# Performance work log

Measured on AMD Instinct MI355X. Metric: run time of the kernel, lower is better.

## Reference

```python
import jax, jax.numpy as jnp
import numpy as np

B, NO, NM, NV, E = 16, 512, 128, 64, 256
H, DK, MS, FF = 16, 16, 8, 512
TRANS_MAX = 100.0


def _ln(x):
    m = x.mean(-1, keepdims=True)
    v = ((x - m) ** 2).mean(-1, keepdims=True)
    return (x - m) * jax.lax.rsqrt(v + 1e-5)


def _inv_norm(x):
    # 1 - minmax-normalize over the whole per-batch matrix
    mn = x.min(axis=(1, 2), keepdims=True)
    mx = x.max(axis=(1, 2), keepdims=True)
    return 1.0 - (x - mn) / (mx - mn)


def _adjacency(proc_time, trans_time, MVpair_trans, mask_dyn, mask_ma):
    # masked copy of proc_time
    A_proc = jnp.where(mask_dyn, proc_time, 0.0)
    # keep only the per-row minimum nonzero entry (min_ProcTime_elements)
    nz = jnp.where(A_proc == 0.0, jnp.inf, A_proc)
    mn = nz.min(axis=2, keepdims=True)
    keep = (A_proc == mn) & (A_proc != 0.0)
    A_proc = A_proc * keep.astype(proc_time.dtype)
    A_proc_norm = (A_proc > 0.0).astype(proc_time.dtype)
    # machine-machine masks
    mask2 = mask_ma[:, None, :] & mask_ma[:, :, None]  # [B, nm, nm]
    A_procing = (~mask2).astype(proc_time.dtype)
    A_off = _inv_norm(MVpair_trans)
    tt = jnp.where(mask2, trans_time, TRANS_MAX + 1.0)
    A_on = _inv_norm(tt)
    return A_proc_norm, A_procing, A_off, A_on


def _block(row, col, cost, Wq, Wk, Wv, Wo, mW1, mb1, mW2, mb2, fW1, fb1, fW2, fb2):
    # MatNet-style mixed-score multi-head attention encoding block
    Bb, R, _ = row.shape
    C = col.shape[1]
    q = (row @ Wq).reshape(Bb, R, H, DK).transpose(0, 2, 1, 3)  # bhrd
    k = (col @ Wk).reshape(Bb, C, H, DK).transpose(0, 2, 1, 3)  # bhcd
    v = (col @ Wv).reshape(Bb, C, H, DK).transpose(0, 2, 1, 3)
    dot = jnp.einsum('bhrd,bhcd->bhrc', q, k) / jnp.sqrt(jnp.asarray(DK, row.dtype))
    two = jnp.stack([dot, jnp.broadcast_to(cost[:, None], dot.shape)], axis=-1)  # [B,H,R,C,2]
    hmix = jax.nn.relu(jnp.einsum('bhrct,hts->bhrcs', two, mW1) + mb1[None, :, None, None, :])
    score = jnp.einsum('bhrcs,hso->bhrco', hmix, mW2)[..., 0] + mb2[:, 0][None, :, None, None]
    attn = jax.nn.softmax(score, axis=-1)
    ctx = jnp.einsum('bhrc,bhcd->bhrd', attn, v).transpose(0, 2, 1, 3).reshape(Bb, R, H * DK)
    out1 = _ln(row + ctx @ Wo)
    ffn = jax.nn.relu(out1 @ fW1 + fb1) @ fW2 + fb2
    return _ln(out1 + ffn)


def setup_inputs() -> dict:
    key = jax.random.key(0)
    ks = jax.random.split(key, 24)

    def nrm(i, shape, s=0.05):
        return jax.random.normal(ks[i], shape, jnp.float32) * s

    return {
        'ope_emb': nrm(0, (B, NO, E), 1.0),
        'ma_emb': nrm(1, (B, NM, E), 1.0),
        'veh_emb': nrm(2, (B, NV, E), 1.0),
        'proc_time': jax.random.uniform(ks[3], (B, NO, NM), jnp.float32) * 20.0,
        'offload_trans_time': jax.random.uniform(ks[4], (B, NO, NV), jnp.float32) * TRANS_MAX,
        'trans_time': jax.random.uniform(ks[5], (B, NM, NM), jnp.float32) * TRANS_MAX,
        'MVpair_trans': jax.random.uniform(ks[6], (B, NV, NM), jnp.float32) * TRANS_MAX,
        'mask_dyn_ope_ma_adj': jax.random.bernoulli(ks[7], 0.3, (B, NO, NM)),
        'mask_ma': jax.random.bernoulli(ks[8], 0.7, (B, NM)),
        # stacked params for the 4 blocks: 0=ope, 1=veh, 2=ma1, 3=ma2
        'Wq': nrm(9, (4, E, H * DK)),
        'Wk': nrm(10, (4, E, H * DK)),
        'Wv': nrm(11, (4, E, H * DK)),
        'Wo': nrm(12, (4, H * DK, E)),
        'mixW1': nrm(13, (4, H, 2, MS), 0.3),
        'mixb1': jnp.zeros((4, H, MS), jnp.float32),
        'mixW2': nrm(14, (4, H, MS, 1), 0.3),
        'mixb2': jnp.zeros((4, H, 1), jnp.float32),
        'ffW1': nrm(15, (4, E, FF)),
        'ffb1': jnp.zeros((4, FF), jnp.float32),
        'ffW2': nrm(16, (4, FF, E)),
        'ffb2': jnp.zeros((4, E), jnp.float32),
        'maprojW': nrm(17, (2 * E, E)),
        'maprojb': jnp.zeros((E,), jnp.float32),
    }


def reference(ope_emb, ma_emb, veh_emb, proc_time, offload_trans_time, trans_time,
              MVpair_trans, mask_dyn_ope_ma_adj, mask_ma,
              Wq, Wk, Wv, Wo, mixW1, mixb1, mixW2, mixb2,
              ffW1, ffb1, ffW2, ffb2, maprojW, maprojb):
    A_proc_norm, A_procing, A_off, A_on = _adjacency(
        proc_time, trans_time, MVpair_trans, mask_dyn_ope_ma_adj, mask_ma)

    def blk(i, row, col, cost):
        return _block(row, col, cost, Wq[i], Wk[i], Wv[i], Wo[i],
                      mixW1[i], mixb1[i], mixW2[i], mixb2[i],
                      ffW1[i], ffb1[i], ffW2[i], ffb2[i])

    ope_out = blk(0, ope_emb, ma_emb, A_proc_norm)
    veh_out = blk(1, veh_emb, ma_emb, A_off)
    ma1 = blk(2, ma_emb, ma_emb, A_procing)
    ma2 = blk(3, ma_emb, ma_emb, A_on)
    ma_out = jnp.concatenate([ma1, ma2], axis=-1) @ maprojW + maprojb
    return (ope_out, ma_out, veh_out)
```

## Files before the change

kernel.cpp:

```cpp
#include <hip/hip_runtime.h>
#include <hip/hip_fp16.h>
#include <hip/hip_bf16.h>


typedef unsigned short u16;
typedef __attribute__((ext_vector_type(8))) short bf16x8;
typedef __attribute__((ext_vector_type(4))) float f32x4;
struct us4 { u16 x, y, z, w; };

__device__ __forceinline__ float bf2f(u16 u) {
  return __uint_as_float(((unsigned int)u) << 16);
}
__device__ __forceinline__ u16 f2bf(float f) {
  unsigned int x = __float_as_uint(f);
  x += 0x7FFFu + ((x >> 16) & 1u);
  return (u16)(x >> 16);
}
__device__ __forceinline__ __half2 h2max(__half2 a, __half2 b) {
  unsigned au = *(unsigned*)&a, bu = *(unsigned*)&b, ru;
  asm("v_pk_max_f16 %0, %1, %2" : "=v"(ru) : "v"(au), "v"(bu));
  return *(__half2*)&ru;
}

#define NBATCH 16
#define NOPE   512
#define NMA    128
#define NVEH   64
#define EDIM   256

struct PrepArgs {
  const float* ope; const float* ma; const float* veh;
  u16* ope_bf; u16* ma_bf; u16* veh_bf;
  const float* proc; const int* mask_dyn; float* A_proc;
  const float* mv; const float* trans; const int* mask_ma;
  unsigned int* mm;
};
struct TrArgs {
  const float* Wq; const float* Wk; const float* Wv; const float* Wo;
  const float* ffW1; const float* ffW2; const float* maproj;
  u16* WqT; u16* WkT; u16* WvT; u16* WoT; u16* ffW1T; u16* ffW2T; u16* maprojT;
};
__global__ __launch_bounds__(256) void prep_a(PrepArgs a, TrArgs tr) {
  int blk = blockIdx.x, t = threadIdx.x;
  if (blk < 2816) {
    int i = blk * 256 + t;
    const float* s; u16* d; int j;
    if (i < 524288)      { s = a.ope; d = a.ope_bf; j = i; }
    else if (i < 655360) { s = a.ma;  d = a.ma_bf;  j = i - 524288; }
    else                 { s = a.veh; d = a.veh_bf; j = i - 655360; }
    float4 v = ((const float4*)s)[j];
    us4 o = { f2bf(v.x), f2bf(v.y), f2bf(v.z), f2bf(v.w) };
    ((us4*)d)[j] = o;
    return;
  }
  if (blk < 6912) {
    int local = blk - 2816;
    int row = local * 2 + (t >> 7);
    int lane = t & 127;
    size_t idx = (size_t)row * NMA + lane;
    float av = a.mask_dyn[idx] ? a.proc[idx] : 0.0f;
    float cand = (av != 0.0f) ? av : 1.0e30f;
    __shared__ float red[256];
    red[t] = cand;
    __syncthreads();
    for (int s = 64; s > 0; s >>= 1) {
      if (lane < s) red[t] = fminf(red[t], red[t + s]);
      __syncthreads();
    }
    float mn = red[t & 128];
    a.A_proc[idx] = (av != 0.0f && av == mn) ? 1.0f : 0.0f;
    return;
  }
  if (blk < 7104) {
    __shared__ float smn[256], smx[256];
    float mn = 1.0e30f, mx = -1.0e30f;
    int mmIdx;
    if (blk < 6976) {
      int local = blk - 6912;
      int b = local >> 2, chunk = local & 3;
      const float* xb = a.mv + (size_t)b * 8192 + chunk * 2048;
#pragma unroll
      for (int r = 0; r < 8; r++) {
        float v = xb[r * 256 + t];
        mn = fminf(mn, v);
        mx = fmaxf(mx, v);
      }
      mmIdx = b;
    } else {
      int local = blk - 6976;
      int b = local >> 3, chunk = local & 7;
      __shared__ unsigned char mrow[NMA];
      if (t < NMA) mrow[t] = (unsigned char)(a.mask_ma[(size_t)b * NMA + t] != 0);
      __syncthreads();
      const float* tb = a.trans + (size_t)b * 16384 + chunk * 2048;
      int rbase = chunk * 16;
#pragma unroll
      for (int r = 0; r < 8; r++) {
        int off = r * 256 + t;
        int row = rbase + (off >> 7), col = off & 127;
        bool m2 = mrow[row] && mrow[col];
        float tt = m2 ? tb[off] : 101.0f;
        mn = fminf(mn, tt);
        mx = fmaxf(mx, tt);
      }
      mmIdx = 16 + b;
    }
    smn[t] = mn; smx[t] = mx;
    __syncthreads();
    for (int s = 128; s > 0; s >>= 1) {
      if (t < s) {
        smn[t] = fminf(smn[t], smn[t + s]);
        smx[t] = fmaxf(smx[t], smx[t + s]);
      }
      __syncthreads();
    }
    if (t == 0) {
      atomicMin(&a.mm[mmIdx], __float_as_uint(smn[0]));
      atomicMax(&a.mm[32 + mmIdx], __float_as_uint(smx[0]));
    }
    return;
  }
  {
    int b2 = blk - 7104;
    const float* src; u16* dst; int Kd, Nd, tile;
    if (b2 < 1024) {
      int w = b2 >> 8, i = (b2 >> 6) & 3; tile = b2 & 63;
      const float* sw = (w == 0 ? tr.Wq : w == 1 ? tr.Wk : w == 2 ? tr.Wv : tr.Wo);
      u16* dw = (w == 0 ? tr.WqT : w == 1 ? tr.WkT : w == 2 ? tr.WvT : tr.WoT);
      src = sw + (size_t)i * 65536; dst = dw + (size_t)i * 65536;
      Kd = 256; Nd = 256;
    } else if (b2 < 1536) {
      int z = (b2 - 1024) >> 7; tile = (b2 - 1024) & 127;
      src = tr.ffW1 + (size_t)z * 131072; dst = tr.ffW1T + (size_t)z * 131072;
      Kd = 256; Nd = 512;
    } else {
      int z = (b2 - 1536) >> 7; tile = (b2 - 1536) & 127;
      if (z < 4) { src = tr.ffW2 + (size_t)z * 131072; dst = tr.ffW2T + (size_t)z * 131072; }
      else       { src = tr.maproj; dst = tr.maprojT; }
      Kd = 512; Nd = 256;
    }
    int nx = Nd >> 5;
    int k0 = (tile / nx) * 32, n0 = (tile % nx) * 32;
    __shared__ float tl[32][33];
    int tx = t & 31, ty = t >> 5;
#pragma unroll
    for (int r = 0; r < 4; r++)
      tl[ty + r * 8][tx] = src[(size_t)(k0 + ty + r * 8) * Nd + n0 + tx];
    __syncthreads();
#pragma unroll
    for (int r = 0; r < 4; r++)
      dst[(size_t)(n0 + ty + r * 8) * Kd + k0 + tx] = f2bf(tl[tx][ty + r * 8]);
  }
}

__global__ __launch_bounds__(256) void prep_b(
    const float* __restrict__ mv, const float* __restrict__ trans,
    const int* __restrict__ mask_ma, const unsigned int* __restrict__ mm,
    float* __restrict__ A_offb, float* __restrict__ a_on,
    float* __restrict__ a_pcing) {
  int blk = blockIdx.x, t = threadIdx.x;
  if (blk < 512) {
    int b = blk >> 5, off = (blk & 31) * 256 + t;
    float lo = __uint_as_float(mm[b]);
    float inv = 1.0f / (__uint_as_float(mm[32 + b]) - lo);
    size_t idx = (size_t)b * 8192 + off;
    A_offb[idx] = 1.0f - (mv[idx] - lo) * inv;
    return;
  }
  int local = blk - 512;
  int b = local >> 6, off = (local & 63) * 256 + t;
  int row = off >> 7, col = off & 127;
  bool m2 = (mask_ma[(size_t)b * NMA + row] != 0) &&
            (mask_ma[(size_t)b * NMA + col] != 0);
  size_t idx = (size_t)b * 16384 + off;
  float tt = m2 ? trans[idx] : 101.0f;
  float lo = __uint_as_float(mm[16 + b]);
  float inv = 1.0f / (__uint_as_float(mm[48 + b]) - lo);
  a_on[idx] = 1.0f - (tt - lo) * inv;
  a_pcing[idx] = m2 ? 0.0f : 1.0f;
}

__global__ __launch_bounds__(256) void transpose_v(
    const u16* __restrict__ src, u16* __restrict__ dst) {
  int g = blockIdx.z >> 4, b = blockIdx.z & 15;
  int d0 = blockIdx.x * 32, c0 = blockIdx.y * 32;
  __shared__ u16 tile[32][33];
  int tx = threadIdx.x & 31, ty = threadIdx.x >> 5;
  const u16* s = src + ((size_t)g * 16 + b) * 32768;
  u16* d = dst + ((size_t)g * 16 + b) * 32768;
#pragma unroll
  for (int r = 0; r < 4; r++)
    tile[ty + r * 8][tx] = s[(size_t)(c0 + ty + r * 8) * 256 + d0 + tx];
  __syncthreads();
#pragma unroll
  for (int r = 0; r < 4; r++)
    d[(size_t)(d0 + ty + r * 8) * 128 + c0 + tx] = tile[tx][ty + r * 8];
}

struct GG {
  const u16* A; const u16* WT; const float* bias; u16* C;
  int M, N, K, epi, wgStart, wgCols, mode;
};
struct GGArgs { GG g[12]; int n; };

__global__ __launch_bounds__(256) void gemm_grouped(GGArgs args) {
  int wg = blockIdx.x;
  int gi = 0;
  for (int i = 1; i < args.n; i++)
    if (wg >= args.g[i].wgStart) gi = i;
  GG gg = args.g[gi];
  int lwg = wg - gg.wgStart;
  int bx = lwg & (gg.wgCols - 1);
  int by = lwg >> ((gg.wgCols == 2) ? 1 : 2);
  int N = gg.N, K = gg.K;

  __shared__ u16 As[128][40];
  __shared__ u16 Bs[128][40];
  int tid = threadIdx.x;
  int lane = tid & 63, wid = tid >> 6;
  int wr = (wid >> 1) * 64, wc = (wid & 1) * 64;
  int m16 = lane & 15, quad = lane >> 4;
  int rb = by * 128, cb = bx * 128;
  int srow = tid >> 2;
  int schunk = (tid & 3) * 8;

  f32x4 acc[4][4];
#pragma unroll
  for (int i = 0; i < 4; i++)
#pragma unroll
    for (int j = 0; j < 4; j++) acc[i][j] = (f32x4){0.f, 0.f, 0.f, 0.f};

  for (int k0 = 0; k0 < K; k0 += 32) {
    uint4 va0 = *(const uint4*)(gg.A + (size_t)(rb + srow) * K + k0 + schunk);
    uint4 va1 = *(const uint4*)(gg.A + (size_t)(rb + 64 + srow) * K + k0 + schunk);
    uint4 vb0 = *(const uint4*)(gg.WT + (size_t)(cb + srow) * K + k0 + schunk);
    uint4 vb1 = *(const uint4*)(gg.WT + (size_t)(cb + 64 + srow) * K + k0 + schunk);
    __syncthreads();
    *(uint4*)&As[srow][schunk] = va0;
    *(uint4*)&As[64 + srow][schunk] = va1;
    *(uint4*)&Bs[srow][schunk] = vb0;
    *(uint4*)&Bs[64 + srow][schunk] = vb1;
    __syncthreads();
    bf16x8 af[4], bfr[4];
#pragma unroll
    for (int i = 0; i < 4; i++)
      af[i] = *(const bf16x8*)&As[wr + i * 16 + m16][quad * 8];
#pragma unroll
    for (int j = 0; j < 4; j++)
      bfr[j] = *(const bf16x8*)&Bs[wc + j * 16 + m16][quad * 8];
#pragma unroll
    for (int i = 0; i < 4; i++)
#pragma unroll
      for (int j = 0; j < 4; j++)
        acc[i][j] = __builtin_amdgcn_mfma_f32_16x16x32_bf16(
            af[i], bfr[j], acc[i][j], 0, 0, 0);
  }

#pragma unroll
  for (int i = 0; i < 4; i++) {
#pragma unroll
    for (int j = 0; j < 4; j++) {
      int col = cb + wc + j * 16 + m16;
      float bv = (gg.epi >= 1) ? gg.bias[col] : 0.0f;
#pragma unroll
      for (int r = 0; r < 4; r++) {
        int row = rb + wr + i * 16 + quad * 4 + r;
        float v = acc[i][j][r] + bv;
        if (gg.epi == 2) v = fmaxf(v, 0.0f);
        size_t off;
        if (gg.mode == 0) {
          off = (size_t)row * N + col;
        } else if (gg.mode == 1) {
          off = ((size_t)(row >> 4)) * 4096 + (size_t)(col >> 4) * 256 +
                (size_t)(row & 15) * 16 + (col & 15);
        } else {
          off = ((size_t)(row >> 7)) * 32768 + (size_t)(col >> 4) * 2048 +
                (size_t)(row & 127) * 16 + (col & 15);
        }
        gg.C[off] = f2bf(v);
      }
    }
  }
}

__global__ __launch_bounds__(256) void gemm_mfma_f32(
    const u16* __restrict__ A, const u16* __restrict__ WT,
    const float* __restrict__ bias, float* __restrict__ C,
    int M, int N, int K) {
  __shared__ u16 As[64][40];
  __shared__ u16 Bs[64][40];
  int tid = threadIdx.x;
  int lane = tid & 63, wid = tid >> 6;
  int wr = (wid >> 1) * 32, wc = (wid & 1) * 32;
  int m16 = lane & 15, quad = lane >> 4;
  int rb = blockIdx.y * 64, cb = blockIdx.x * 64;
  int srow = tid >> 2;
  int schunk = (tid & 3) * 8;
  f32x4 acc[2][2];
#pragma unroll
  for (int i = 0; i < 2; i++)
#pragma unroll
    for (int j = 0; j < 2; j++) acc[i][j] = (f32x4){0.f, 0.f, 0.f, 0.f};
  for (int k0 = 0; k0 < K; k0 += 32) {
    uint4 va = *(const uint4*)(A + (size_t)(rb + srow) * K + k0 + schunk);
    uint4 vb = *(const uint4*)(WT + (size_t)(cb + srow) * K + k0 + schunk);
    __syncthreads();
    *(uint4*)&As[srow][schunk] = va;
    *(uint4*)&Bs[srow][schunk] = vb;
    __syncthreads();
    bf16x8 af[2], bfr[2];
#pragma unroll
    for (int i = 0; i < 2; i++)
      af[i] = *(const bf16x8*)&As[wr + i * 16 + m16][quad * 8];
#pragma unroll
    for (int j = 0; j < 2; j++)
      bfr[j] = *(const bf16x8*)&Bs[wc + j * 16 + m16][quad * 8];
#pragma unroll
    for (int i = 0; i < 2; i++)
#pragma unroll
      for (int j = 0; j < 2; j++)
        acc[i][j] = __builtin_amdgcn_mfma_f32_16x16x32_bf16(
            af[i], bfr[j], acc[i][j], 0, 0, 0);
  }
#pragma unroll
  for (int i = 0; i < 2; i++)
#pragma unroll
    for (int j = 0; j < 2; j++) {
      int col = cb + wc + j * 16 + m16;
      float bv = bias[col];
#pragma unroll
      for (int r = 0; r < 4; r++) {
        int row = rb + wr + i * 16 + quad * 4 + r;
        C[(size_t)row * N + col] = acc[i][j][r] + bv;
      }
    }
}

struct AG {
  const u16* q; const u16* k; const u16* vT; const float* cost; u16* ctx;
  const float* w1; const float* b1; const float* w2; const float* b2;
  int R, wgStart;
};
struct AGArgs { AG g[4]; };

#define CSTRIDE 134

__global__ __launch_bounds__(256) void attn_grouped(AGArgs args) {
  int blk = blockIdx.x;
  int gi = 0;
#pragma unroll
  for (int i = 1; i < 4; i++)
    if (blk >= args.g[i].wgStart) gi = i;
  AG gg = args.g[gi];
  int local = blk - gg.wgStart;

  int t = threadIdx.x;
  int wave = t >> 6, lane = t & 63;
  int quad = lane >> 4, l16 = lane & 15;
  int j = local & 15;
  int b = (j & 7) * 2 + (j >> 3);
  int hgrp = (local >> 4) & 1;
  int tile = local >> 5;
  int m0 = b * gg.R + tile * 16;

  __shared__ __half costs_h[16 * CSTRIDE];
  __shared__ u16 pbuf[4][16 * 136];

  const float* cp = gg.cost + (size_t)m0 * 128;
  for (int i = t; i < 2048; i += 256)
    costs_h[(i >> 7) * CSTRIDE + (i & 127)] = __float2half(cp[i]);
  __syncthreads();

  const bf16x8 zerof = (bf16x8){0, 0, 0, 0, 0, 0, 0, 0};
  const f32x4 zacc = (f32x4){0.f, 0.f, 0.f, 0.f};
  const __half2 zh = __float2half2_rn(0.0f);
  u16* pb = pbuf[wave];
  const u16* qtile = gg.q + ((size_t)(m0 >> 4)) * 4096;
  const u16* kb    = gg.k + (size_t)b * 32768;

#pragma unroll
  for (int hh = 0; hh < 2; hh++) {
    int h = hgrp * 8 + wave * 2 + hh;

    __half2 w10h[8], w11h[8], b1h[8], w2h[8];
#pragma unroll
    for (int s = 0; s < 8; s++) {
      w10h[s] = __float2half2_rn(gg.w1[h * 16 + s] * 0.25f);
      w11h[s] = __float2half2_rn(gg.w1[h * 16 + 8 + s]);
      b1h[s]  = __float2half2_rn(gg.b1[h * 8 + s]);
      w2h[s]  = __float2half2_rn(gg.w2[h * 8 + s]);
    }
    float wb2v = gg.b2[h];

    bf16x8 bq = zerof;
    if (quad < 2)
      bq = *(const bf16x8*)(qtile + (size_t)h * 256 + l16 * 16 + quad * 8);
    f32x4 st[8];
    __builtin_amdgcn_s_setprio(1);
#pragma unroll
    for (int ct = 0; ct < 8; ct++) {
      bf16x8 ak = zerof;
      if (quad < 2)
        ak = *(const bf16x8*)(kb + (size_t)h * 2048 + (ct * 16 + l16) * 16 +
                              quad * 8);
      st[ct] = __builtin_amdgcn_mfma_f32_16x16x32_bf16(ak, bq, zacc, 0, 0, 0);
    }
    __builtin_amdgcn_s_setprio(0);

#pragma unroll
    for (int ct = 0; ct < 8; ct++) {
#pragma unroll
      for (int p = 0; p < 2; p++) {
        __half2 d2 = __float22half2_rn(
            make_float2(st[ct][p * 2], st[ct][p * 2 + 1]));
        __half2 c2 = *(const __half2*)&costs_h[l16 * CSTRIDE + ct * 16 +
                                               quad * 4 + p * 2];
        __half2 s2 = zh;
#pragma unroll
        for (int s = 0; s < 8; s++) {
          __half2 hm = __hfma2(d2, w10h[s], __hfma2(c2, w11h[s], b1h[s]));
          hm = h2max(hm, zh);
          s2 = __hfma2(hm, w2h[s], s2);
        }
        float2 sf = __half22float2(s2);
        st[ct][p * 2]     = sf.x + wb2v;
        st[ct][p * 2 + 1] = sf.y + wb2v;
      }
    }

    float mx = -1.0e30f;
#pragma unroll
    for (int ct = 0; ct < 8; ct++)
#pragma unroll
      for (int rg = 0; rg < 4; rg++) mx = fmaxf(mx, st[ct][rg]);
    mx = fmaxf(mx, __shfl_xor(mx, 16, 64));
    mx = fmaxf(mx, __shfl_xor(mx, 32, 64));
    float sum = 0.0f;
#pragma unroll
    for (int ct = 0; ct < 8; ct++)
#pragma unroll
      for (int rg = 0; rg < 4; rg++) {
        float e = __expf(st[ct][rg] - mx);
        st[ct][rg] = e;
        sum += e;
      }
    sum += __shfl_xor(sum, 16, 64);
    sum += __shfl_xor(sum, 32, 64);
    float inv = 1.0f / sum;

#pragma unroll
    for (int ct = 0; ct < 8; ct++) {
#pragma unroll
      for (int p = 0; p < 2; p++) {
        __hip_bfloat162 pk = __float22bfloat162_rn(
            make_float2(st[ct][p * 2] * inv, st[ct][p * 2 + 1] * inv));
        *(unsigned int*)&pb[l16 * 136 + ct * 16 + quad * 4 + p * 2] =
            *(unsigned int*)&pk;
      }
    }

    f32x4 cacc = zacc;
    __builtin_amdgcn_s_setprio(1);
#pragma unroll
    for (int ks = 0; ks < 4; ks++) {
      bf16x8 ap = *(const bf16x8*)&pb[l16 * 136 + ks * 32 + quad * 8];
      bf16x8 bv = *(const bf16x8*)(gg.vT + (size_t)b * 32768 +
                                   (size_t)(h * 16 + l16) * 128 + ks * 32 +
                                   quad * 8);
      cacc = __builtin_amdgcn_mfma_f32_16x16x32_bf16(ap, bv, cacc, 0, 0, 0);
    }
    __builtin_amdgcn_s_setprio(0);

#pragma unroll
    for (int rg = 0; rg < 4; rg++)
      gg.ctx[(size_t)(m0 + quad * 4 + rg) * 256 + h * 16 + l16] =
          f2bf(cacc[rg]);
  }
}

struct LN1Args {
  const float* r0; const float* r1; const float* r2; const float* r3;
  int s1, s2, s3;
};
__global__ __launch_bounds__(256) void ln1_grouped(
    LN1Args a, const u16* __restrict__ x, u16* __restrict__ out) {
  int row = blockIdx.x * 4 + (threadIdx.x >> 6);
  int lane = threadIdx.x & 63;
  const float* resid;
  int local;
  if (row < a.s1)      { resid = a.r0; local = row; }
  else if (row < a.s2) { resid = a.r1; local = row - a.s1; }
  else if (row < a.s3) { resid = a.r2; local = row - a.s2; }
  else                 { resid = a.r3; local = row - a.s3; }
  float4 rv = *(const float4*)(resid + (size_t)local * 256 + lane * 4);
  us4 xv = *(const us4*)(x + (size_t)row * 256 + lane * 4);
  float v0 = rv.x + bf2f(xv.x);
  float v1 = rv.y + bf2f(xv.y);
  float v2 = rv.z + bf2f(xv.z);
  float v3 = rv.w + bf2f(xv.w);
  float s  = v0 + v1 + v2 + v3;
  float ss = v0 * v0 + v1 * v1 + v2 * v2 + v3 * v3;
#pragma unroll
  for (int d = 1; d < 64; d <<= 1) {
    s  += __shfl_xor(s, d, 64);
    ss += __shfl_xor(ss, d, 64);
  }
  float mean = s * (1.0f / 256.0f);
  float var = ss * (1.0f / 256.0f) - mean * mean;
  float rs = rsqrtf(fmaxf(var, 0.0f) + 1e-5f);
  us4 o = { f2bf((v0 - mean) * rs), f2bf((v1 - mean) * rs),
            f2bf((v2 - mean) * rs), f2bf((v3 - mean) * rs) };
  *(us4*)(out + (size_t)row * 256 + lane * 4) = o;
}

struct LN2Args {
  float* f0; float* f1; u16* b2; u16* b3;
  int s1, s2, s3;
};
__global__ __launch_bounds__(256) void ln2_grouped(
    LN2Args a, const u16* __restrict__ resid, const u16* __restrict__ x) {
  int row = blockIdx.x * 4 + (threadIdx.x >> 6);
  int lane = threadIdx.x & 63;
  us4 rv = *(const us4*)(resid + (size_t)row * 256 + lane * 4);
  us4 xv = *(const us4*)(x + (size_t)row * 256 + lane * 4);
  float v0 = bf2f(rv.x) + bf2f(xv.x);
  float v1 = bf2f(rv.y) + bf2f(xv.y);
  float v2 = bf2f(rv.z) + bf2f(xv.z);
  float v3 = bf2f(rv.w) + bf2f(xv.w);
  float s  = v0 + v1 + v2 + v3;
  float ss = v0 * v0 + v1 * v1 + v2 * v2 + v3 * v3;
#pragma unroll
  for (int d = 1; d < 64; d <<= 1) {
    s  += __shfl_xor(s, d, 64);
    ss += __shfl_xor(ss, d, 64);
  }
  float mean = s * (1.0f / 256.0f);
  float var = ss * (1.0f / 256.0f) - mean * mean;
  float rs = rsqrtf(fmaxf(var, 0.0f) + 1e-5f);
  float y0 = (v0 - mean) * rs, y1 = (v1 - mean) * rs;
  float y2 = (v2 - mean) * rs, y3 = (v3 - mean) * rs;
  if (row < a.s1) {
    float4 o = {y0, y1, y2, y3};
    *(float4*)(a.f0 + (size_t)row * 256 + lane * 4) = o;
  } else if (row < a.s2) {
    float4 o = {y0, y1, y2, y3};
    *(float4*)(a.f1 + (size_t)(row - a.s1) * 256 + lane * 4) = o;
  } else if (row < a.s3) {
    us4 o = { f2bf(y0), f2bf(y1), f2bf(y2), f2bf(y3) };
    *(us4*)(a.b2 + (size_t)(row - a.s2) * 512 + lane * 4) = o;
  } else {
    us4 o = { f2bf(y0), f2bf(y1), f2bf(y2), f2bf(y3) };
    *(us4*)(a.b3 + (size_t)(row - a.s3) * 512 + 256 + lane * 4) = o;
  }
}

extern "C" void kernel_launch(void* const* d_in, const int* in_sizes, int n_in,
                              void* d_out, int out_size, void* d_ws, size_t ws_size,
                              hipStream_t stream) {
  const float* ope   = (const float*)d_in[0];
  const float* ma    = (const float*)d_in[1];
  const float* veh   = (const float*)d_in[2];
  const float* proc  = (const float*)d_in[3];
  const float* trans = (const float*)d_in[5];
  const float* mv    = (const float*)d_in[6];
  const int* mask_dyn = (const int*)d_in[7];
  const int* mask_ma  = (const int*)d_in[8];
  const float* Wq = (const float*)d_in[9];
  const float* Wk = (const float*)d_in[10];
  const float* Wv = (const float*)d_in[11];
  const float* Wo = (const float*)d_in[12];
  const float* mixW1 = (const float*)d_in[13];
  const float* mixb1 = (const float*)d_in[14];
  const float* mixW2 = (const float*)d_in[15];
  const float* mixb2 = (const float*)d_in[16];
  const float* ffW1 = (const float*)d_in[17];
  const float* ffb1 = (const float*)d_in[18];
  const float* ffW2 = (const float*)d_in[19];
  const float* ffb2 = (const float*)d_in[20];
  const float* maprojW = (const float*)d_in[21];
  const float* maprojb = (const float*)d_in[22];
  float* out = (float*)d_out;
  char* ws = (char*)d_ws;

  const int OFF[4] = {0, 8192, 9216, 11264};
  const int MS4[4] = {8192, 1024, 2048, 2048};
  const int TOT = 13312;

  const size_t MB = 1 << 20;
  float* A_proc  = (float*)(ws + 0);
  float* A_offb  = (float*)(ws + 4 * MB);
  float* A_pcing = (float*)(ws + 4 * MB + MB / 2);
  float* A_on    = (float*)(ws + 5 * MB + MB / 2);
  u16* ope_bf  = (u16*)(ws + 6 * MB + MB / 2);
  u16* ma_bf   = (u16*)(ws + 10 * MB + MB / 2);
  u16* veh_bf  = (u16*)(ws + 11 * MB + MB / 2);
  u16* WqT     = (u16*)(ws + 12 * MB);
  u16* WkT     = (u16*)(ws + 12 * MB + MB / 2);
  u16* WvT     = (u16*)(ws + 13 * MB);
  u16* WoT     = (u16*)(ws + 13 * MB + MB / 2);
  u16* ffW1T   = (u16*)(ws + 14 * MB);
  u16* ffW2T   = (u16*)(ws + 15 * MB);
  u16* maprojT = (u16*)(ws + 16 * MB);
  u16* q_all   = (u16*)(ws + 16 * MB + MB / 2);
  u16* k_all   = (u16*)(ws + 23 * MB);
  u16* v_all   = (u16*)(ws + 27 * MB);
  u16* vT_all  = (u16*)(ws + 31 * MB);
  u16* ctx_all = (u16*)(ws + 35 * MB);
  u16* t1_all  = (u16*)(ws + 41 * MB + MB / 2);
  u16* out1_all= (u16*)(ws + 48 * MB);
  u16* ffh_all = (u16*)(ws + 54 * MB + MB / 2);
  u16* maCat   = (u16*)(ws + 67 * MB + MB / 2);
  unsigned int* mmbuf = (unsigned int*)(ws + 70 * MB);

  hipMemsetAsync(mmbuf, 0x7F, 128, stream);
  hipMemsetAsync((char*)mmbuf + 128, 0x00, 128, stream);

  {
    PrepArgs pa = {ope, ma, veh, ope_bf, ma_bf, veh_bf,
                   proc, mask_dyn, A_proc, mv, trans, mask_ma, mmbuf};
    TrArgs ta = {Wq, Wk, Wv, Wo, ffW1, ffW2, maprojW,
                 WqT, WkT, WvT, WoT, ffW1T, ffW2T, maprojT};
    prep_a<<<9280, 256, 0, stream>>>(pa, ta);
  }

  prep_b<<<1536, 256, 0, stream>>>(mv, trans, mask_ma, mmbuf,
                                   A_offb, A_on, A_pcing);

  const size_t MA_OUT  = (size_t)NBATCH * NOPE * EDIM;
  const size_t VEH_OUT = MA_OUT + (size_t)NBATCH * NMA * EDIM;

  const u16* rowbf[4] = {ope_bf, veh_bf, ma_bf, ma_bf};
  const float* costp[4] = {A_proc, A_offb, A_pcing, A_on};

  {
    GGArgs ga; ga.n = 12;
    int wg = 0;
    for (int i = 0; i < 4; i++) {
      ga.g[i] = {rowbf[i], WqT + (size_t)i * 65536, nullptr,
                 q_all + (size_t)OFF[i] * 256, MS4[i], 256, 256, 0, wg, 2, 1};
      wg += (MS4[i] / 128) * 2;
    }
    for (int i = 0; i < 4; i++) {
      ga.g[4 + i] = {ma_bf, WkT + (size_t)i * 65536, nullptr,
                     k_all + (size_t)i * 524288, 2048, 256, 256, 0, wg, 2, 2};
      wg += 32;
    }
    for (int i = 0; i < 4; i++) {
      ga.g[8 + i] = {ma_bf, WvT + (size_t)i * 65536, nullptr,
                     v_all + (size_t)i * 524288, 2048, 256, 256, 0, wg, 2, 0};
      wg += 32;
    }
    gemm_grouped<<<wg, 256, 0, stream>>>(ga);
  }

  transpose_v<<<dim3(8, 4, 64), 256, 0, stream>>>(v_all, vT_all);

  {
    AGArgs aa;
    int wg = 0;
    const int R4[4] = {NOPE, NVEH, NMA, NMA};
    for (int i = 0; i < 4; i++) {
      aa.g[i] = {q_all + (size_t)OFF[i] * 256, k_all + (size_t)i * 524288,
                 vT_all + (size_t)i * 524288, costp[i],
                 ctx_all + (size_t)OFF[i] * 256,
                 mixW1 + (size_t)i * 256, mixb1 + (size_t)i * 128,
                 mixW2 + (size_t)i * 128, mixb2 + (size_t)i * 16,
                 R4[i], wg};
      wg += MS4[i] / 8;
    }
    attn_grouped<<<wg, 256, 0, stream>>>(aa);
  }

  {
    GGArgs ga; ga.n = 4;
    int wg = 0;
    for (int i = 0; i < 4; i++) {
      ga.g[i] = {ctx_all + (size_t)OFF[i] * 256, WoT + (size_t)i * 65536,
                 nullptr, t1_all + (size_t)OFF[i] * 256,
                 MS4[i], 256, 256, 0, wg, 2, 0};
      wg += (MS4[i] / 128) * 2;
    }
    gemm_grouped<<<wg, 256, 0, stream>>>(ga);
  }

  {
    LN1Args la = {ope, veh, ma, ma, 8192, 9216, 11264};
    ln1_grouped<<<TOT / 4, 256, 0, stream>>>(la, t1_all, out1_all);
  }

  {
    GGArgs ga; ga.n = 4;
    int wg = 0;
    for (int i = 0; i < 4; i++) {
      ga.g[i] = {out1_all + (size_t)OFF[i] * 256, ffW1T + (size_t)i * 131072,
                 ffb1 + (size_t)i * 512, ffh_all + (size_t)OFF[i] * 512,
                 MS4[i], 512, 256, 2, wg, 4, 0};
      wg += (MS4[i] / 128) * 4;
    }
    gemm_grouped<<<wg, 256, 0, stream>>>(ga);
  }

  {
    GGArgs ga; ga.n = 4;
    int wg = 0;
    for (int i = 0; i < 4; i++) {
      ga.g[i] = {ffh_all + (size_t)OFF[i] * 512, ffW2T + (size_t)i * 131072,
                 ffb2 + (size_t)i * 256, t1_all + (size_t)OFF[i] * 256,
                 MS4[i], 256, 512, 1, wg, 2, 0};
      wg += (MS4[i] / 128) * 2;
    }
    gemm_grouped<<<wg, 256, 0, stream>>>(ga);
  }

  {
    LN2Args la = {out, out + VEH_OUT, maCat, maCat, 8192, 9216, 11264};
    ln2_grouped<<<TOT / 4, 256, 0, stream>>>(la, out1_all, t1_all);
  }

  gemm_mfma_f32<<<dim3(4, 32), 256, 0, stream>>>(maCat, maprojT, maprojb,
      out + MA_OUT, 2048, 256, 512);
}
```

Before: 250.7 us.

## Fold prep_b and V transpose into grouped GEMM, switch to 64x64 tiles

The grouped GEMM now uses 64x64 output tiles with a 128-wide K chunk per shared-memory stage, replacing the 128x128 tile with 32-wide K steps. This gives more workgroups and fewer barriers per K. The V projection writes its transposed layout directly from the epilogue, which removes the transpose_v kernel and the intermediate v_all buffer. The prep_b cost-matrix work runs as extra workgroups appended to the first grouped GEMM launch, and the final maproj GEMM reuses the grouped kernel with a float-output mode. Together these remove three launches, at the price of less register-level reuse per tile and scattered 8-byte writes for V.

Result: slower. 354.8 us (+41.5%).

```diff
diff --git a/kernel.cpp b/kernel.cpp
--- a/kernel.cpp
+++ b/kernel.cpp
@@ -153,187 +153,135 @@
   }
 }
 
-__global__ __launch_bounds__(256) void prep_b(
-    const float* __restrict__ mv, const float* __restrict__ trans,
-    const int* __restrict__ mask_ma, const unsigned int* __restrict__ mm,
-    float* __restrict__ A_offb, float* __restrict__ a_on,
-    float* __restrict__ a_pcing) {
-  int blk = blockIdx.x, t = threadIdx.x;
+struct PB {
+  const float* mv; const float* trans; const int* mask_ma;
+  const unsigned int* mm; float* A_offb; float* a_on; float* a_pcing;
+};
+__device__ __forceinline__ void prep_b_body(const PB& p, int blk, int t) {
   if (blk < 512) {
     int b = blk >> 5, off = (blk & 31) * 256 + t;
-    float lo = __uint_as_float(mm[b]);
-    float inv = 1.0f / (__uint_as_float(mm[32 + b]) - lo);
+    float lo = __uint_as_float(p.mm[b]);
+    float inv = 1.0f / (__uint_as_float(p.mm[32 + b]) - lo);
     size_t idx = (size_t)b * 8192 + off;
-    A_offb[idx] = 1.0f - (mv[idx] - lo) * inv;
+    p.A_offb[idx] = 1.0f - (p.mv[idx] - lo) * inv;
     return;
   }
   int local = blk - 512;
   int b = local >> 6, off = (local & 63) * 256 + t;
   int row = off >> 7, col = off & 127;
-  bool m2 = (mask_ma[(size_t)b * NMA + row] != 0) &&
-            (mask_ma[(size_t)b * NMA + col] != 0);
+  bool m2 = (p.mask_ma[(size_t)b * NMA + row] != 0) &&
+            (p.mask_ma[(size_t)b * NMA + col] != 0);
   size_t idx = (size_t)b * 16384 + off;
-  float tt = m2 ? trans[idx] : 101.0f;
-  float lo = __uint_as_float(mm[16 + b]);
-  float inv = 1.0f / (__uint_as_float(mm[48 + b]) - lo);
-  a_on[idx] = 1.0f - (tt - lo) * inv;
-  a_pcing[idx] = m2 ? 0.0f : 1.0f;
-}
-
-__global__ __launch_bounds__(256) void transpose_v(
-    const u16* __restrict__ src, u16* __restrict__ dst) {
-  int g = blockIdx.z >> 4, b = blockIdx.z & 15;
-  int d0 = blockIdx.x * 32, c0 = blockIdx.y * 32;
-  __shared__ u16 tile[32][33];
-  int tx = threadIdx.x & 31, ty = threadIdx.x >> 5;
-  const u16* s = src + ((size_t)g * 16 + b) * 32768;
-  u16* d = dst + ((size_t)g * 16 + b) * 32768;
-#pragma unroll
-  for (int r = 0; r < 4; r++)
-    tile[ty + r * 8][tx] = s[(size_t)(c0 + ty + r * 8) * 256 + d0 + tx];
-  __syncthreads();
-#pragma unroll
-  for (int r = 0; r < 4; r++)
-    d[(size_t)(d0 + ty + r * 8) * 128 + c0 + tx] = tile[tx][ty + r * 8];
+  float tt = m2 ? p.trans[idx] : 101.0f;
+  float lo = __uint_as_float(p.mm[16 + b]);
+  float inv = 1.0f / (__uint_as_float(p.mm[48 + b]) - lo);
+  p.a_on[idx] = 1.0f - (tt - lo) * inv;
+  p.a_pcing[idx] = m2 ? 0.0f : 1.0f;
 }
 
 struct GG {
   const u16* A; const u16* WT; const float* bias; u16* C;
-  int M, N, K, epi, wgStart, wgCols, mode;
+  int M, N, K, epi, wgStart, cshift, mode;
 };
-struct GGArgs { GG g[12]; int n; };
+struct GGArgs { GG g[12]; PB pb; int n; int nGemmWG; };
 
 __global__ __launch_bounds__(256) void gemm_grouped(GGArgs args) {
   int wg = blockIdx.x;
+  if (wg >= args.nGemmWG) {
+    prep_b_body(args.pb, wg - args.nGemmWG, threadIdx.x);
+    return;
+  }
   int gi = 0;
   for (int i = 1; i < args.n; i++)
     if (wg >= args.g[i].wgStart) gi = i;
   GG gg = args.g[gi];
   int lwg = wg - gg.wgStart;
-  int bx = lwg & (gg.wgCols - 1);
-  int by = lwg >> ((gg.wgCols == 2) ? 1 : 2);
+  int bx = lwg & ((1 << gg.cshift) - 1);
+  int by = lwg >> gg.cshift;
   int N = gg.N, K = gg.K;
 
-  __shared__ u16 As[128][40];
-  __shared__ u16 Bs[128][40];
-  int tid = threadIdx.x;
-  int lane = tid & 63, wid = tid >> 6;
-  int wr = (wid >> 1) * 64, wc = (wid & 1) * 64;
-  int m16 = lane & 15, quad = lane >> 4;
-  int rb = by * 128, cb = bx * 128;
-  int srow = tid >> 2;
-  int schunk = (tid & 3) * 8;
-
-  f32x4 acc[4][4];
-#pragma unroll
-  for (int i = 0; i < 4; i++)
-#pragma unroll
-    for (int j = 0; j < 4; j++) acc[i][j] = (f32x4){0.f, 0.f, 0.f, 0.f};
-
-  for (int k0 = 0; k0 < K; k0 += 32) {
-    uint4 va0 = *(const uint4*)(gg.A + (size_t)(rb + srow) * K + k0 + schunk);
-    uint4 va1 = *(const uint4*)(gg.A + (size_t)(rb + 64 + srow) * K + k0 + schunk);
-    uint4 vb0 = *(const uint4*)(gg.WT + (size_t)(cb + srow) * K + k0 + schunk);
-    uint4 vb1 = *(const uint4*)(gg.WT + (size_t)(cb + 64 + srow) * K + k0 + schunk);
-    __syncthreads();
-    *(uint4*)&As[srow][schunk] = va0;
-    *(uint4*)&As[64 + srow][schunk] = va1;
-    *(uint4*)&Bs[srow][schunk] = vb0;
-    *(uint4*)&Bs[64 + srow][schunk] = vb1;
-    __syncthreads();
-    bf16x8 af[4], bfr[4];
-#pragma unroll
-    for (int i = 0; i < 4; i++)
-      af[i] = *(const bf16x8*)&As[wr + i * 16 + m16][quad * 8];
-#pragma unroll
-    for (int j = 0; j < 4; j++)
-      bfr[j] = *(const bf16x8*)&Bs[wc + j * 16 + m16][quad * 8];
-#pragma unroll
-    for (int i = 0; i < 4; i++)
-#pragma unroll
-      for (int j = 0; j < 4; j++)
-        acc[i][j] = __builtin_amdgcn_mfma_f32_16x16x32_bf16(
-            af[i], bfr[j], acc[i][j], 0, 0, 0);
-  }
-
-#pragma unroll
-  for (int i = 0; i < 4; i++) {
-#pragma unroll
-    for (int j = 0; j < 4; j++) {
-      int col = cb + wc + j * 16 + m16;
-      float bv = (gg.epi >= 1) ? gg.bias[col] : 0.0f;
-#pragma unroll
-      for (int r = 0; r < 4; r++) {
-        int row = rb + wr + i * 16 + quad * 4 + r;
-        float v = acc[i][j][r] + bv;
-        if (gg.epi == 2) v = fmaxf(v, 0.0f);
-        size_t off;
-        if (gg.mode == 0) {
-          off = (size_t)row * N + col;
-        } else if (gg.mode == 1) {
-          off = ((size_t)(row >> 4)) * 4096 + (size_t)(col >> 4) * 256 +
-                (size_t)(row & 15) * 16 + (col & 15);
-        } else {
-          off = ((size_t)(row >> 7)) * 32768 + (size_t)(col >> 4) * 2048 +
-                (size_t)(row & 127) * 16 + (col & 15);
-        }
-        gg.C[off] = f2bf(v);
-      }
-    }
-  }
-}
-
-__global__ __launch_bounds__(256) void gemm_mfma_f32(
-    const u16* __restrict__ A, const u16* __restrict__ WT,
-    const float* __restrict__ bias, float* __restrict__ C,
-    int M, int N, int K) {
-  __shared__ u16 As[64][40];
-  __shared__ u16 Bs[64][40];
+  __shared__ u16 As[64][136];
+  __shared__ u16 Bs[64][136];
   int tid = threadIdx.x;
   int lane = tid & 63, wid = tid >> 6;
   int wr = (wid >> 1) * 32, wc = (wid & 1) * 32;
   int m16 = lane & 15, quad = lane >> 4;
-  int rb = blockIdx.y * 64, cb = blockIdx.x * 64;
+  int rb = by * 64, cb = bx * 64;
   int srow = tid >> 2;
   int schunk = (tid & 3) * 8;
+
   f32x4 acc[2][2];
 #pragma unroll
   for (int i = 0; i < 2; i++)
 #pragma unroll
     for (int j = 0; j < 2; j++) acc[i][j] = (f32x4){0.f, 0.f, 0.f, 0.f};
-  for (int k0 = 0; k0 < K; k0 += 32) {
-    uint4 va = *(const uint4*)(A + (size_t)(rb + srow) * K + k0 + schunk);
-    uint4 vb = *(const uint4*)(WT + (size_t)(cb + srow) * K + k0 + schunk);
+
+  for (int kc = 0; kc < K; kc += 128) {
+    uint4 va[4], vb[4];
+    const u16* ap = gg.A + (size_t)(rb + srow) * K + kc + schunk;
+    const u16* bp = gg.WT + (size_t)(cb + srow) * K + kc + schunk;
+#pragma unroll
+    for (int c = 0; c < 4; c++) {
+      va[c] = *(const uint4*)(ap + c * 32);
+      vb[c] = *(const uint4*)(bp + c * 32);
+    }
     __syncthreads();
-    *(uint4*)&As[srow][schunk] = va;
-    *(uint4*)&Bs[srow][schunk] = vb;
+#pragma unroll
+    for (int c = 0; c < 4; c++) {
+      *(uint4*)&As[srow][c * 32 + schunk] = va[c];
+      *(uint4*)&Bs[srow][c * 32 + schunk] = vb[c];
+    }
     __syncthreads();
-    bf16x8 af[2], bfr[2];
-#pragma unroll
-    for (int i = 0; i < 2; i++)
-      af[i] = *(const bf16x8*)&As[wr + i * 16 + m16][quad * 8];
-#pragma unroll
-    for (int j = 0; j < 2; j++)
-      bfr[j] = *(const bf16x8*)&Bs[wc + j * 16 + m16][quad * 8];
-#pragma unroll
-    for (int i = 0; i < 2; i++)
-#pragma unroll
-      for (int j = 0; j < 2; j++)
-        acc[i][j] = __builtin_amdgcn_mfma_f32_16x16x32_bf16(
-            af[i], bfr[j], acc[i][j], 0, 0, 0);
-  }
-#pragma unroll
-  for (int i = 0; i < 2; i++)
+#pragma unroll
+    for (int ks = 0; ks < 4; ks++) {
+      bf16x8 af0 = *(const bf16x8*)&As[wr + m16][ks * 32 + quad * 8];
+      bf16x8 af1 = *(const bf16x8*)&As[wr + 16 + m16][ks * 32 + quad * 8];
+      bf16x8 bf0 = *(const bf16x8*)&Bs[wc + m16][ks * 32 + quad * 8];
+      bf16x8 bf1 = *(const bf16x8*)&Bs[wc + 16 + m16][ks * 32 + quad * 8];
+      acc[0][0] = __builtin_amdgcn_mfma_f32_16x16x32_bf16(af0, bf0, acc[0][0], 0, 0, 0);
+      acc[0][1] = __builtin_amdgcn_mfma_f32_16x16x32_bf16(af0, bf1, acc[0][1], 0, 0, 0);
+      acc[1][0] = __builtin_amdgcn_mfma_f32_16x16x32_bf16(af1, bf0, acc[1][0], 0, 0, 0);
+      acc[1][1] = __builtin_amdgcn_mfma_f32_16x16x32_bf16(af1, bf1, acc[1][1], 0, 0, 0);
+    }
+  }
+
+#pragma unroll
+  for (int i = 0; i < 2; i++) {
 #pragma unroll
     for (int j = 0; j < 2; j++) {
       int col = cb + wc + j * 16 + m16;
-      float bv = bias[col];
-#pragma unroll
-      for (int r = 0; r < 4; r++) {
-        int row = rb + wr + i * 16 + quad * 4 + r;
-        C[(size_t)row * N + col] = acc[i][j][r] + bv;
+      float bv = (gg.epi >= 1) ? gg.bias[col] : 0.0f;
+      if (gg.mode == 3) {
+        int row0 = rb + wr + i * 16 + quad * 4;
+        int b = row0 >> 7, c0 = row0 & 127;
+        us4 o = { f2bf(acc[i][j][0]), f2bf(acc[i][j][1]),
+                  f2bf(acc[i][j][2]), f2bf(acc[i][j][3]) };
+        *(us4*)(gg.C + (size_t)b * 32768 + (size_t)col * 128 + c0) = o;
+      } else {
+#pragma unroll
+        for (int r = 0; r < 4; r++) {
+          int row = rb + wr + i * 16 + quad * 4 + r;
+          float v = acc[i][j][r] + bv;
+          if (gg.epi == 2) v = fmaxf(v, 0.0f);
+          if (gg.mode == 4) {
+            ((float*)gg.C)[(size_t)row * N + col] = v;
+          } else {
+            size_t off;
+            if (gg.mode == 0) {
+              off = (size_t)row * N + col;
+            } else if (gg.mode == 1) {
+              off = ((size_t)(row >> 4)) * 4096 + (size_t)(col >> 4) * 256 +
+                    (size_t)(row & 15) * 16 + (col & 15);
+            } else {
+              off = ((size_t)(row >> 7)) * 32768 + (size_t)(col >> 4) * 2048 +
+                    (size_t)(row & 127) * 16 + (col & 15);
+            }
+            gg.C[off] = f2bf(v);
+          }
+        }
       }
     }
+  }
 }
 
 struct AG {
@@ -603,7 +551,6 @@
   u16* maprojT = (u16*)(ws + 16 * MB);
   u16* q_all   = (u16*)(ws + 16 * MB + MB / 2);
   u16* k_all   = (u16*)(ws + 23 * MB);
-  u16* v_all   = (u16*)(ws + 27 * MB);
   u16* vT_all  = (u16*)(ws + 31 * MB);
   u16* ctx_all = (u16*)(ws + 35 * MB);
   u16* t1_all  = (u16*)(ws + 41 * MB + MB / 2);
@@ -623,37 +570,34 @@
     prep_a<<<9280, 256, 0, stream>>>(pa, ta);
   }
 
-  prep_b<<<1536, 256, 0, stream>>>(mv, trans, mask_ma, mmbuf,
-                                   A_offb, A_on, A_pcing);
-
   const size_t MA_OUT  = (size_t)NBATCH * NOPE * EDIM;
   const size_t VEH_OUT = MA_OUT + (size_t)NBATCH * NMA * EDIM;
 
   const u16* rowbf[4] = {ope_bf, veh_bf, ma_bf, ma_bf};
   const float* costp[4] = {A_proc, A_offb, A_pcing, A_on};
-
-  {
-    GGArgs ga; ga.n = 12;
+  PB pb = {mv, trans, mask_ma, mmbuf, A_offb, A_on, A_pcing};
+
+  {
+    GGArgs ga; ga.n = 12; ga.pb = pb;
     int wg = 0;
     for (int i = 0; i < 4; i++) {
       ga.g[i] = {rowbf[i], WqT + (size_t)i * 65536, nullptr,
                  q_all + (size_t)OFF[i] * 256, MS4[i], 256, 256, 0, wg, 2, 1};
-      wg += (MS4[i] / 128) * 2;
+      wg += (MS4[i] / 64) * 4;
     }
     for (int i = 0; i < 4; i++) {
       ga.g[4 + i] = {ma_bf, WkT + (size_t)i * 65536, nullptr,
                      k_all + (size_t)i * 524288, 2048, 256, 256, 0, wg, 2, 2};
-      wg += 32;
+      wg += 32 * 4;
     }
     for (int i = 0; i < 4; i++) {
       ga.g[8 + i] = {ma_bf, WvT + (size_t)i * 65536, nullptr,
-                     v_all + (size_t)i * 524288, 2048, 256, 256, 0, wg, 2, 0};
-      wg += 32;
-    }
-    gemm_grouped<<<wg, 256, 0, stream>>>(ga);
-  }
-
-  transpose_v<<<dim3(8, 4, 64), 256, 0, stream>>>(v_all, vT_all);
+                     vT_all + (size_t)i * 524288, 2048, 256, 256, 0, wg, 2, 3};
+      wg += 32 * 4;
+    }
+    ga.nGemmWG = wg;
+    gemm_grouped<<<wg + 1536, 256, 0, stream>>>(ga);
+  }
 
   {
     AGArgs aa;
@@ -672,14 +616,15 @@
   }
 
   {
-    GGArgs ga; ga.n = 4;
+    GGArgs ga; ga.n = 4; ga.pb = pb;
     int wg = 0;
     for (int i = 0; i < 4; i++) {
       ga.g[i] = {ctx_all + (size_t)OFF[i] * 256, WoT + (size_t)i * 65536,
                  nullptr, t1_all + (size_t)OFF[i] * 256,
                  MS4[i], 256, 256, 0, wg, 2, 0};
-      wg += (MS4[i] / 128) * 2;
-    }
+      wg += (MS4[i] / 64) * 4;
+    }
+    ga.nGemmWG = wg;
     gemm_grouped<<<wg, 256, 0, stream>>>(ga);
   }
 
@@ -689,26 +634,28 @@
   }
 
   {
-    GGArgs ga; ga.n = 4;
+    GGArgs ga; ga.n = 4; ga.pb = pb;
     int wg = 0;
     for (int i = 0; i < 4; i++) {
       ga.g[i] = {out1_all + (size_t)OFF[i] * 256, ffW1T + (size_t)i * 131072,
                  ffb1 + (size_t)i * 512, ffh_all + (size_t)OFF[i] * 512,
-                 MS4[i], 512, 256, 2, wg, 4, 0};
-      wg += (MS4[i] / 128) * 4;
-    }
+                 MS4[i], 512, 256, 2, wg, 3, 0};
+      wg += (MS4[i] / 64) * 8;
+    }
+    ga.nGemmWG = wg;
     gemm_grouped<<<wg, 256, 0, stream>>>(ga);
   }
 
   {
-    GGArgs ga; ga.n = 4;
+    GGArgs ga; ga.n = 4; ga.pb = pb;
     int wg = 0;
     for (int i = 0; i < 4; i++) {
       ga.g[i] = {ffh_all + (size_t)OFF[i] * 512, ffW2T + (size_t)i * 131072,
                  ffb2 + (size_t)i * 256, t1_all + (size_t)OFF[i] * 256,
                  MS4[i], 256, 512, 1, wg, 2, 0};
-      wg += (MS4[i] / 128) * 2;
-    }
+      wg += (MS4[i] / 64) * 4;
+    }
+    ga.nGemmWG = wg;
     gemm_grouped<<<wg, 256, 0, stream>>>(ga);
   }
 
@@ -717,6 +664,11 @@
     ln2_grouped<<<TOT / 4, 256, 0, stream>>>(la, out1_all, t1_all);
   }
 
-  gemm_mfma_f32<<<dim3(4, 32), 256, 0, stream>>>(maCat, maprojT, maprojb,
-      out + MA_OUT, 2048, 256, 512);
-}
+  {
+    GGArgs ga; ga.n = 1; ga.pb = pb;
+    ga.g[0] = {maCat, maprojT, maprojb, (u16*)(out + MA_OUT),
+               2048, 256, 512, 1, 0, 2, 4};
+    ga.nGemmWG = 128;
+    gemm_grouped<<<128, 256, 0, stream>>>(ga);
+  }
+}
```

## Fuse V transpose into QKV GEMM epilogue and fold prep_b into grouped GEMM

Applied to the files above, without the earlier changes.

Adds an epilogue mode to the grouped GEMM that writes V directly in transposed per-batch layout, removing the separate transpose_v kernel and its extra round trip through global memory. The prep_b work (A_off, A_on, A_procing normalization) is appended as extra workgroups to the QKV grouped GEMM launch, saving another kernel launch and letting that elementwise work overlap the GEMM tiles. The column-index decode changes from a wgCols mask to a shift parameter. The transposed stores are 8-byte scattered writes with stride 128 across columns, which may coalesce less well than the original row-major writes.

After: 252.9 us. Within noise of the previous version (+0.9%).

```diff
diff --git a/kernel.cpp b/kernel.cpp
--- a/kernel.cpp
+++ b/kernel.cpp
@@ -153,65 +153,51 @@
   }
 }
 
-__global__ __launch_bounds__(256) void prep_b(
-    const float* __restrict__ mv, const float* __restrict__ trans,
-    const int* __restrict__ mask_ma, const unsigned int* __restrict__ mm,
-    float* __restrict__ A_offb, float* __restrict__ a_on,
-    float* __restrict__ a_pcing) {
-  int blk = blockIdx.x, t = threadIdx.x;
+struct PB {
+  const float* mv; const float* trans; const int* mask_ma;
+  const unsigned int* mm; float* A_offb; float* a_on; float* a_pcing;
+};
+__device__ __forceinline__ void prep_b_body(const PB& p, int blk, int t) {
   if (blk < 512) {
     int b = blk >> 5, off = (blk & 31) * 256 + t;
-    float lo = __uint_as_float(mm[b]);
-    float inv = 1.0f / (__uint_as_float(mm[32 + b]) - lo);
+    float lo = __uint_as_float(p.mm[b]);
+    float inv = 1.0f / (__uint_as_float(p.mm[32 + b]) - lo);
     size_t idx = (size_t)b * 8192 + off;
-    A_offb[idx] = 1.0f - (mv[idx] - lo) * inv;
+    p.A_offb[idx] = 1.0f - (p.mv[idx] - lo) * inv;
     return;
   }
   int local = blk - 512;
   int b = local >> 6, off = (local & 63) * 256 + t;
   int row = off >> 7, col = off & 127;
-  bool m2 = (mask_ma[(size_t)b * NMA + row] != 0) &&
-            (mask_ma[(size_t)b * NMA + col] != 0);
+  bool m2 = (p.mask_ma[(size_t)b * NMA + row] != 0) &&
+            (p.mask_ma[(size_t)b * NMA + col] != 0);
   size_t idx = (size_t)b * 16384 + off;
-  float tt = m2 ? trans[idx] : 101.0f;
-  float lo = __uint_as_float(mm[16 + b]);
-  float inv = 1.0f / (__uint_as_float(mm[48 + b]) - lo);
-  a_on[idx] = 1.0f - (tt - lo) * inv;
-  a_pcing[idx] = m2 ? 0.0f : 1.0f;
-}
-
-__global__ __launch_bounds__(256) void transpose_v(
-    const u16* __restrict__ src, u16* __restrict__ dst) {
-  int g = blockIdx.z >> 4, b = blockIdx.z & 15;
-  int d0 = blockIdx.x * 32, c0 = blockIdx.y * 32;
-  __shared__ u16 tile[32][33];
-  int tx = threadIdx.x & 31, ty = threadIdx.x >> 5;
-  const u16* s = src + ((size_t)g * 16 + b) * 32768;
-  u16* d = dst + ((size_t)g * 16 + b) * 32768;
-#pragma unroll
-  for (int r = 0; r < 4; r++)
-    tile[ty + r * 8][tx] = s[(size_t)(c0 + ty + r * 8) * 256 + d0 + tx];
-  __syncthreads();
-#pragma unroll
-  for (int r = 0; r < 4; r++)
-    d[(size_t)(d0 + ty + r * 8) * 128 + c0 + tx] = tile[tx][ty + r * 8];
+  float tt = m2 ? p.trans[idx] : 101.0f;
+  float lo = __uint_as_float(p.mm[16 + b]);
+  float inv = 1.0f / (__uint_as_float(p.mm[48 + b]) - lo);
+  p.a_on[idx] = 1.0f - (tt - lo) * inv;
+  p.a_pcing[idx] = m2 ? 0.0f : 1.0f;
 }
 
 struct GG {
   const u16* A; const u16* WT; const float* bias; u16* C;
-  int M, N, K, epi, wgStart, wgCols, mode;
+  int M, N, K, epi, wgStart, cshift, mode;
 };
-struct GGArgs { GG g[12]; int n; };
+struct GGArgs { GG g[12]; PB pb; int n; int nGemmWG; };
 
 __global__ __launch_bounds__(256) void gemm_grouped(GGArgs args) {
   int wg = blockIdx.x;
+  if (wg >= args.nGemmWG) {
+    prep_b_body(args.pb, wg - args.nGemmWG, threadIdx.x);
+    return;
+  }
   int gi = 0;
   for (int i = 1; i < args.n; i++)
     if (wg >= args.g[i].wgStart) gi = i;
   GG gg = args.g[gi];
   int lwg = wg - gg.wgStart;
-  int bx = lwg & (gg.wgCols - 1);
-  int by = lwg >> ((gg.wgCols == 2) ? 1 : 2);
+  int bx = lwg & ((1 << gg.cshift) - 1);
+  int by = lwg >> gg.cshift;
   int N = gg.N, K = gg.K;
 
   __shared__ u16 As[128][40];
@@ -262,22 +248,30 @@
     for (int j = 0; j < 4; j++) {
       int col = cb + wc + j * 16 + m16;
       float bv = (gg.epi >= 1) ? gg.bias[col] : 0.0f;
-#pragma unroll
-      for (int r = 0; r < 4; r++) {
-        int row = rb + wr + i * 16 + quad * 4 + r;
-        float v = acc[i][j][r] + bv;
-        if (gg.epi == 2) v = fmaxf(v, 0.0f);
-        size_t off;
-        if (gg.mode == 0) {
-          off = (size_t)row * N + col;
-        } else if (gg.mode == 1) {
-          off = ((size_t)(row >> 4)) * 4096 + (size_t)(col >> 4) * 256 +
-                (size_t)(row & 15) * 16 + (col & 15);
-        } else {
-          off = ((size_t)(row >> 7)) * 32768 + (size_t)(col >> 4) * 2048 +
-                (size_t)(row & 127) * 16 + (col & 15);
+      if (gg.mode == 3) {
+        int row0 = rb + wr + i * 16 + quad * 4;
+        int b = row0 >> 7, c0 = row0 & 127;
+        us4 o = { f2bf(acc[i][j][0]), f2bf(acc[i][j][1]),
+                  f2bf(acc[i][j][2]), f2bf(acc[i][j][3]) };
+        *(us4*)(gg.C + (size_t)b * 32768 + (size_t)col * 128 + c0) = o;
+      } else {
+#pragma unroll
+        for (int r = 0; r < 4; r++) {
+          int row = rb + wr + i * 16 + quad * 4 + r;
+          float v = acc[i][j][r] + bv;
+          if (gg.epi == 2) v = fmaxf(v, 0.0f);
+          size_t off;
+          if (gg.mode == 0) {
+            off = (size_t)row * N + col;
+          } else if (gg.mode == 1) {
+            off = ((size_t)(row >> 4)) * 4096 + (size_t)(col >> 4) * 256 +
+                  (size_t)(row & 15) * 16 + (col & 15);
+          } else {
+            off = ((size_t)(row >> 7)) * 32768 + (size_t)(col >> 4) * 2048 +
+                  (size_t)(row & 127) * 16 + (col & 15);
+          }
+          gg.C[off] = f2bf(v);
         }
-        gg.C[off] = f2bf(v);
       }
     }
   }
@@ -603,7 +597,6 @@
   u16* maprojT = (u16*)(ws + 16 * MB);
   u16* q_all   = (u16*)(ws + 16 * MB + MB / 2);
   u16* k_all   = (u16*)(ws + 23 * MB);
-  u16* v_all   = (u16*)(ws + 27 * MB);
   u16* vT_all  = (u16*)(ws + 31 * MB);
   u16* ctx_all = (u16*)(ws + 35 * MB);
   u16* t1_all  = (u16*)(ws + 41 * MB + MB / 2);
@@ -623,37 +616,34 @@
     prep_a<<<9280, 256, 0, stream>>>(pa, ta);
   }
 
-  prep_b<<<1536, 256, 0, stream>>>(mv, trans, mask_ma, mmbuf,
-                                   A_offb, A_on, A_pcing);
-
   const size_t MA_OUT  = (size_t)NBATCH * NOPE * EDIM;
   const size_t VEH_OUT = MA_OUT + (size_t)NBATCH * NMA * EDIM;
 
   const u16* rowbf[4] = {ope_bf, veh_bf, ma_bf, ma_bf};
   const float* costp[4] = {A_proc, A_offb, A_pcing, A_on};
-
-  {
-    GGArgs ga; ga.n = 12;
+  PB pb = {mv, trans, mask_ma, mmbuf, A_offb, A_on, A_pcing};
+
+  {
+    GGArgs ga; ga.n = 12; ga.pb = pb;
     int wg = 0;
     for (int i = 0; i < 4; i++) {
       ga.g[i] = {rowbf[i], WqT + (size_t)i * 65536, nullptr,
-                 q_all + (size_t)OFF[i] * 256, MS4[i], 256, 256, 0, wg, 2, 1};
+                 q_all + (size_t)OFF[i] * 256, MS4[i], 256, 256, 0, wg, 1, 1};
       wg += (MS4[i] / 128) * 2;
     }
     for (int i = 0; i < 4; i++) {
       ga.g[4 + i] = {ma_bf, WkT + (size_t)i * 65536, nullptr,
-                     k_all + (size_t)i * 524288, 2048, 256, 256, 0, wg, 2, 2};
+                     k_all + (size_t)i * 524288, 2048, 256, 256, 0, wg, 1, 2};
       wg += 32;
     }
     for (int i = 0; i < 4; i++) {
       ga.g[8 + i] = {ma_bf, WvT + (size_t)i * 65536, nullptr,
-                     v_all + (size_t)i * 524288, 2048, 256, 256, 0, wg, 2, 0};
+                     vT_all + (size_t)i * 524288, 2048, 256, 256, 0, wg, 1, 3};
       wg += 32;
     }
-    gemm_grouped<<<wg, 256, 0, stream>>>(ga);
-  }
-
-  transpose_v<<<dim3(8, 4, 64), 256, 0, stream>>>(v_all, vT_all);
+    ga.nGemmWG = wg;
+    gemm_grouped<<<wg + 1536, 256, 0, stream>>>(ga);
+  }
 
   {
     AGArgs aa;
@@ -672,14 +662,15 @@
   }
 
   {
-    GGArgs ga; ga.n = 4;
+    GGArgs ga; ga.n = 4; ga.pb = pb;
     int wg = 0;
     for (int i = 0; i < 4; i++) {
       ga.g[i] = {ctx_all + (size_t)OFF[i] * 256, WoT + (size_t)i * 65536,
                  nullptr, t1_all + (size_t)OFF[i] * 256,
-                 MS4[i], 256, 256, 0, wg, 2, 0};
+                 MS4[i], 256, 256, 0, wg, 1, 0};
       wg += (MS4[i] / 128) * 2;
     }
+    ga.nGemmWG = wg;
     gemm_grouped<<<wg, 256, 0, stream>>>(ga);
   }
 
@@ -689,26 +680,28 @@
   }
 
   {
-    GGArgs ga; ga.n = 4;
+    GGArgs ga; ga.n = 4; ga.pb = pb;
     int wg = 0;
     for (int i = 0; i < 4; i++) {
       ga.g[i] = {out1_all + (size_t)OFF[i] * 256, ffW1T + (size_t)i * 131072,
                  ffb1 + (size_t)i * 512, ffh_all + (size_t)OFF[i] * 512,
-                 MS4[i], 512, 256, 2, wg, 4, 0};
+                 MS4[i], 512, 256, 2, wg, 2, 0};
       wg += (MS4[i] / 128) * 4;
     }
+    ga.nGemmWG = wg;
     gemm_grouped<<<wg, 256, 0, stream>>>(ga);
   }
 
   {
-    GGArgs ga; ga.n = 4;
+    GGArgs ga; ga.n = 4; ga.pb = pb;
     int wg = 0;
     for (int i = 0; i < 4; i++) {
       ga.g[i] = {ffh_all + (size_t)OFF[i] * 512, ffW2T + (size_t)i * 131072,
                  ffb2 + (size_t)i * 256, t1_all + (size_t)OFF[i] * 256,
-                 MS4[i], 256, 512, 1, wg, 2, 0};
+                 MS4[i], 256, 512, 1, wg, 1, 0};
       wg += (MS4[i] / 128) * 2;
     }
+    ga.nGemmWG = wg;
     gemm_grouped<<<wg, 256, 0, stream>>>(ga);
   }
 
```
